# Kernel tuning notes

Hardware: AMD Instinct MI355X
Metric: run time of the kernel (lower is better)

Reference implementation:

```python
import jax, jax.numpy as jnp
import numpy as np

N_NODES = 50000
N_EDGES = 800000
D_FEAT = 64


def setup_inputs() -> dict:
    key = jax.random.key(0)
    k_x, k_e, k_w = jax.random.split(key, 3)
    x = jax.random.normal(k_x, (N_NODES, D_FEAT), dtype=jnp.float32)
    edge_index = jax.random.randint(k_e, (2, N_EDGES), 0, N_NODES, dtype=jnp.int64)
    # message MLP params (phi_Theta): single linear + ReLU
    W = jax.random.normal(k_w, (D_FEAT, D_FEAT), dtype=jnp.float32) / np.sqrt(D_FEAT)
    b = jnp.zeros((D_FEAT,), dtype=jnp.float32)
    return {"x": x, "edge_index": edge_index, "W": W, "b": b}


def reference(x, edge_index, W, b):
    # flow = source_to_target: messages flow from edge_index[0] (j) to edge_index[1] (i)
    src = edge_index[0]  # j: source nodes (gather)
    dst = edge_index[1]  # i: target nodes (scatter index)
    n_nodes = x.shape[0]
    # __collect__: index_select gather of source node features -> x_j [E, D]
    x_j = x[src]
    # message: per-edge MLP  phi(x_j) = relu(x_j W + b)
    msg = jax.nn.relu(jnp.einsum('ed,df->ef', x_j, W) + b)
    # aggregate: scatter-add into target nodes (aggr='add', dim_size = size_i)
    out = jax.ops.segment_sum(msg, dst, num_segments=n_nodes)
    # update: identity
    return out
```

## Files before the change

kernel.cpp:

```cpp
#include <hip/hip_runtime.h>
#include <hip/hip_bf16.h>

#define D 64
#define CAP 32
#define OVF_CAP 16384
#define NSHARD 8

__device__ __forceinline__ float bf2f(unsigned short u) {
    return __uint_as_float((unsigned int)u << 16);
}
__device__ __forceinline__ unsigned short f2bf(float f) {
    unsigned int u = __float_as_uint(f);
    unsigned int r = (u + 0x7fffu + ((u >> 16) & 1u)) >> 16;
    return (unsigned short)r;
}

__global__ __launch_bounds__(256) void node_mlp_kernel(
    const float* __restrict__ x, const float* __restrict__ W,
    const float* __restrict__ b, unsigned short* __restrict__ m0,
    unsigned short* __restrict__ m1, int* __restrict__ cnt,
    int* __restrict__ ovf_cnt, int n_nodes) {
    for (int i = blockIdx.x * blockDim.x + threadIdx.x; i < n_nodes;
         i += gridDim.x * blockDim.x) cnt[i] = 0;
    if (blockIdx.x == 0 && threadIdx.x == 0) *ovf_cnt = 0;

    const int lane = threadIdx.x & 63;
    const int l31 = lane & 31;
    unsigned short* mp = (lane < 32) ? m0 : m1;
    float w[D];
    #pragma unroll
    for (int k = 0; k < D; ++k) w[k] = W[k * D + lane];
    const float bias = b[lane];

    const int wave = (blockIdx.x * blockDim.x + threadIdx.x) >> 6;
    const int nwaves = (gridDim.x * blockDim.x) >> 6;

    for (int row = wave; row < n_nodes; row += nwaves) {
        const float4* xr = (const float4*)(x + (size_t)row * D);
        float acc = bias;
        #pragma unroll
        for (int kk = 0; kk < D / 4; ++kk) {
            float4 xv = xr[kk];
            acc = fmaf(xv.x, w[4 * kk + 0], acc);
            acc = fmaf(xv.y, w[4 * kk + 1], acc);
            acc = fmaf(xv.z, w[4 * kk + 2], acc);
            acc = fmaf(xv.w, w[4 * kk + 3], acc);
        }
        mp[(size_t)row * 32 + l31] = f2bf(fmaxf(acc, 0.0f));
    }
}

__global__ __launch_bounds__(256) void append_kernel(
    const int* __restrict__ src, const int* __restrict__ dst,
    int* __restrict__ cnt, unsigned short* __restrict__ slots,
    int* __restrict__ ovf_cnt, unsigned int* __restrict__ ovf,
    int n_edges, int blocks_per_shard) {
    const int shard = blockIdx.x & (NSHARD - 1);
    const int p = blockIdx.x >> 3;
    const int chunk = (n_edges + blocks_per_shard - 1) / blocks_per_shard;
    const int beg = p * chunk;
    const int end = min(beg + chunk, n_edges);

    for (int e = beg + (int)threadIdx.x; e < end; e += 256) {
        int d = dst[e];
        if ((d & (NSHARD - 1)) != shard) continue;
        int s = src[e];
        int pos = atomicAdd(&cnt[d], 1);
        if (pos < CAP) {
            slots[(size_t)d * CAP + pos] = (unsigned short)s;
        } else {
            int op = atomicAdd(ovf_cnt, 1);
            if (op < OVF_CAP)
                ovf[op] = ((unsigned int)d << 16) | (unsigned int)s;
        }
    }
}

__global__ __launch_bounds__(256) void gather_pass_kernel(
    const unsigned short* __restrict__ slots, const int* __restrict__ cnt,
    const unsigned short* __restrict__ m0, const unsigned short* __restrict__ m1,
    const int* __restrict__ ovf_cnt, const unsigned int* __restrict__ ovf,
    float* __restrict__ out, int n_nodes, int gblocks) {
    const int plane = ((int)blockIdx.x >= gblocks) ? 1 : 0;
    const int blk = (int)blockIdx.x - plane * gblocks;
    const unsigned short* mplane = plane ? m1 : m0;
    const int col0 = plane * 32;

    const int lane = threadIdx.x & 63;
    const int l31 = lane & 31;
    const int wave = (blk * 256 + (int)threadIdx.x) >> 6;
    const int node = wave * 2 + ((lane >> 5) & 1);
    if (node >= n_nodes) return;

    const int c = cnt[node];
    const int cc = min(c, CAP);
    unsigned int idx = (unsigned int)slots[(size_t)node * CAP + l31];
    const int bsel = lane & 32;

    float acc = 0.0f;
    int k = 0;
    for (; k + 4 <= cc; k += 4) {
        unsigned int s0 = __shfl(idx, bsel + k + 0);
        unsigned int s1 = __shfl(idx, bsel + k + 1);
        unsigned int s2 = __shfl(idx, bsel + k + 2);
        unsigned int s3 = __shfl(idx, bsel + k + 3);
        float v0 = bf2f(mplane[(size_t)s0 * 32 + l31]);
        float v1 = bf2f(mplane[(size_t)s1 * 32 + l31]);
        float v2 = bf2f(mplane[(size_t)s2 * 32 + l31]);
        float v3 = bf2f(mplane[(size_t)s3 * 32 + l31]);
        acc += (v0 + v1) + (v2 + v3);
    }
    for (; k < cc; ++k) {
        unsigned int s = __shfl(idx, bsel + k);
        acc += bf2f(mplane[(size_t)s * 32 + l31]);
    }
    if (c > CAP) {
        int oc = min(*ovf_cnt, OVF_CAP);
        for (int i = 0; i < oc; ++i) {
            unsigned int e = ovf[i];
            if ((int)(e >> 16) == node)
                acc += bf2f(mplane[(size_t)(e & 0xFFFFu) * 32 + l31]);
        }
    }
    out[(size_t)node * D + col0 + l31] = acc;
}

__global__ __launch_bounds__(256) void edge_scatter_kernel(
    const int* __restrict__ src, const int* __restrict__ dst,
    const unsigned short* __restrict__ m0, const unsigned short* __restrict__ m1,
    float* __restrict__ out, int n_edges) {
    long long t = (long long)blockIdx.x * blockDim.x + threadIdx.x;
    int e = (int)(t >> 4);
    if (e >= n_edges) return;
    int c = (int)(t & 15) << 2;
    int s = src[e];
    int d = dst[e];
    const unsigned short* mp = (c < 32) ? m0 : m1;
    const ushort4 v = *(const ushort4*)(mp + (size_t)s * 32 + (c & 31));
    float* o = out + (size_t)d * D + c;
    atomicAdd(o + 0, bf2f(v.x));
    atomicAdd(o + 1, bf2f(v.y));
    atomicAdd(o + 2, bf2f(v.z));
    atomicAdd(o + 3, bf2f(v.w));
}

static inline size_t align_up(size_t v, size_t a) { return (v + a - 1) & ~(a - 1); }

extern "C" void kernel_launch(void* const* d_in, const int* in_sizes, int n_in,
                              void* d_out, int out_size, void* d_ws, size_t ws_size,
                              hipStream_t stream) {
    const float* x = (const float*)d_in[0];
    const int* edge_index = (const int*)d_in[1];
    const float* W = (const float*)d_in[2];
    const float* b = (const float*)d_in[3];
    float* out = (float*)d_out;

    const int n_nodes = in_sizes[0] / D;
    const int n_edges = in_sizes[1] / 2;
    const int* src = edge_index;
    const int* dst = edge_index + n_edges;

    size_t off = 0;
    unsigned short* m0 = (unsigned short*)((char*)d_ws + off);
    off = align_up(off + (size_t)n_nodes * 32 * sizeof(unsigned short), 256);
    unsigned short* m1 = (unsigned short*)((char*)d_ws + off);
    off = align_up(off + (size_t)n_nodes * 32 * sizeof(unsigned short), 256);
    int* cnt = (int*)((char*)d_ws + off);
    off = align_up(off + (size_t)n_nodes * sizeof(int), 256);
    unsigned short* slots = (unsigned short*)((char*)d_ws + off);
    off = align_up(off + (size_t)n_nodes * CAP * sizeof(unsigned short), 256);
    int* ovf_cnt = (int*)((char*)d_ws + off);
    off = align_up(off + sizeof(int), 256);
    unsigned int* ovf = (unsigned int*)((char*)d_ws + off);
    off = align_up(off + (size_t)OVF_CAP * sizeof(unsigned int), 256);
    const size_t needed = off;

    node_mlp_kernel<<<512, 256, 0, stream>>>(x, W, b, m0, m1, cnt, ovf_cnt, n_nodes);

    if (ws_size >= needed && n_nodes <= 65536) {
        const int blocks_per_shard = 128;
        append_kernel<<<blocks_per_shard * NSHARD, 256, 0, stream>>>(
            src, dst, cnt, slots, ovf_cnt, ovf, n_edges, blocks_per_shard);
        const int gblocks = (n_nodes + 7) / 8;
        gather_pass_kernel<<<gblocks * 2, 256, 0, stream>>>(
            slots, cnt, m0, m1, ovf_cnt, ovf, out, n_nodes, gblocks);
    } else {
        hipMemsetAsync(d_out, 0, (size_t)out_size * sizeof(float), stream);
        long long total_threads = (long long)n_edges * 16;
        int scat_blocks = (int)((total_threads + 255) / 256);
        edge_scatter_kernel<<<scat_blocks, 256, 0, stream>>>(src, dst, m0, m1,
                                                             out, n_edges);
    }
}
```

Baseline: 158.3 us.

## Gather one node per wave across both planes with uniform slot loads

The gather kernel now maps one node to a full 64-lane wave, with the lower half reading plane m0 and the upper half plane m1. Before, each half-wave handled a different node in a single plane, with a separate launch range per plane. Because the node index is wave-uniform (readfirstlane), the slot indices can be read as packed 32-bit scalar loads instead of a per-lane load followed by shuffles. The main loop is unrolled to 8 neighbours for more memory parallelism. Each slot row is now read once instead of twice, and the output row is written as one contiguous 64-wide store, at the cost of wave-uniform trip counts and more registers.

```diff
diff --git a/kernel.cpp b/kernel.cpp
--- a/kernel.cpp
+++ b/kernel.cpp
@@ -76,42 +76,48 @@
     }
 }
 
-__global__ __launch_bounds__(256) void gather_pass_kernel(
+__global__ __launch_bounds__(256) void gather_kernel(
     const unsigned short* __restrict__ slots, const int* __restrict__ cnt,
     const unsigned short* __restrict__ m0, const unsigned short* __restrict__ m1,
     const int* __restrict__ ovf_cnt, const unsigned int* __restrict__ ovf,
-    float* __restrict__ out, int n_nodes, int gblocks) {
-    const int plane = ((int)blockIdx.x >= gblocks) ? 1 : 0;
-    const int blk = (int)blockIdx.x - plane * gblocks;
-    const unsigned short* mplane = plane ? m1 : m0;
-    const int col0 = plane * 32;
+    float* __restrict__ out, int n_nodes) {
+    int node = blockIdx.x * 4 + (threadIdx.x >> 6);
+    if (node >= n_nodes) return;
+    node = __builtin_amdgcn_readfirstlane(node);
 
     const int lane = threadIdx.x & 63;
     const int l31 = lane & 31;
-    const int wave = (blk * 256 + (int)threadIdx.x) >> 6;
-    const int node = wave * 2 + ((lane >> 5) & 1);
-    if (node >= n_nodes) return;
+    const unsigned short* __restrict__ mplane = (lane < 32) ? m0 : m1;
 
     const int c = cnt[node];
     const int cc = min(c, CAP);
-    unsigned int idx = (unsigned int)slots[(size_t)node * CAP + l31];
-    const int bsel = lane & 32;
+    const unsigned int* __restrict__ row =
+        (const unsigned int*)(slots + (size_t)node * CAP);
 
     float acc = 0.0f;
     int k = 0;
-    for (; k + 4 <= cc; k += 4) {
-        unsigned int s0 = __shfl(idx, bsel + k + 0);
-        unsigned int s1 = __shfl(idx, bsel + k + 1);
-        unsigned int s2 = __shfl(idx, bsel + k + 2);
-        unsigned int s3 = __shfl(idx, bsel + k + 3);
+    for (; k + 8 <= cc; k += 8) {
+        unsigned int p0 = row[(k >> 1) + 0];
+        unsigned int p1 = row[(k >> 1) + 1];
+        unsigned int p2 = row[(k >> 1) + 2];
+        unsigned int p3 = row[(k >> 1) + 3];
+        unsigned int s0 = p0 & 0xFFFFu, s1 = p0 >> 16;
+        unsigned int s2 = p1 & 0xFFFFu, s3 = p1 >> 16;
+        unsigned int s4 = p2 & 0xFFFFu, s5 = p2 >> 16;
+        unsigned int s6 = p3 & 0xFFFFu, s7 = p3 >> 16;
         float v0 = bf2f(mplane[(size_t)s0 * 32 + l31]);
         float v1 = bf2f(mplane[(size_t)s1 * 32 + l31]);
         float v2 = bf2f(mplane[(size_t)s2 * 32 + l31]);
         float v3 = bf2f(mplane[(size_t)s3 * 32 + l31]);
-        acc += (v0 + v1) + (v2 + v3);
+        float v4 = bf2f(mplane[(size_t)s4 * 32 + l31]);
+        float v5 = bf2f(mplane[(size_t)s5 * 32 + l31]);
+        float v6 = bf2f(mplane[(size_t)s6 * 32 + l31]);
+        float v7 = bf2f(mplane[(size_t)s7 * 32 + l31]);
+        acc += ((v0 + v1) + (v2 + v3)) + ((v4 + v5) + (v6 + v7));
     }
     for (; k < cc; ++k) {
-        unsigned int s = __shfl(idx, bsel + k);
+        unsigned int p = row[k >> 1];
+        unsigned int s = (k & 1) ? (p >> 16) : (p & 0xFFFFu);
         acc += bf2f(mplane[(size_t)s * 32 + l31]);
     }
     if (c > CAP) {
@@ -122,7 +128,7 @@
                 acc += bf2f(mplane[(size_t)(e & 0xFFFFu) * 32 + l31]);
         }
     }
-    out[(size_t)node * D + col0 + l31] = acc;
+    out[(size_t)node * D + lane] = acc;
 }
 
 __global__ __launch_bounds__(256) void edge_scatter_kernel(
@@ -181,9 +187,8 @@
         const int blocks_per_shard = 128;
         append_kernel<<<blocks_per_shard * NSHARD, 256, 0, stream>>>(
             src, dst, cnt, slots, ovf_cnt, ovf, n_edges, blocks_per_shard);
-        const int gblocks = (n_nodes + 7) / 8;
-        gather_pass_kernel<<<gblocks * 2, 256, 0, stream>>>(
-            slots, cnt, m0, m1, ovf_cnt, ovf, out, n_nodes, gblocks);
+        gather_kernel<<<(n_nodes + 3) / 4, 256, 0, stream>>>(
+            slots, cnt, m0, m1, ovf_cnt, ovf, out, n_nodes);
     } else {
         hipMemsetAsync(d_out, 0, (size_t)out_size * sizeof(float), stream);
         long long total_threads = (long long)n_edges * 16;
```

Result: no change. 160.9 us (+1.6%).
